# Kernel tuning notes

Hardware: AMD Instinct MI355X
Metric: run time of the kernel (lower is better)

## Reference

```python
import jax, jax.numpy as jnp
import numpy as np
from jax import lax

K = 3; KK = K * K; S = 1; P = 1; D = 1
BN_EPS = 1e-5


def setup_inputs() -> dict:
    key = jax.random.key(0)
    ks = jax.random.split(key, 4)
    B, C, H, W = 8, 128, 64, 64
    cout = 128
    # xavier-ish scales for conv weights
    def xavier(k, shape):
        fan_in = shape[1] * shape[2] * shape[3]
        fan_out = shape[0] * shape[2] * shape[3]
        limit = np.sqrt(6.0 / (fan_in + fan_out))
        return jax.random.uniform(k, shape, jnp.float32, -limit, limit)
    return {
        "x": jax.random.normal(ks[0], (B, C, H, W), jnp.float32),
        "w_off": xavier(ks[1], (2 * KK, C, K, K)),
        "b_off": jnp.zeros((2 * KK,), jnp.float32),
        "w_mod": xavier(ks[2], (KK, C, K, K)),
        "b_mod": jnp.zeros((KK,), jnp.float32),
        "w_reg": xavier(ks[3], (cout, C, K, K)),
        "b_reg": jnp.zeros((cout,), jnp.float32),
        "gamma": jnp.ones((cout,), jnp.float32),
        "beta": jnp.zeros((cout,), jnp.float32),
    }


def _conv(x, w, b):
    y = lax.conv_general_dilated(x, w, (S, S), [(P, P), (P, P)],
                                 rhs_dilation=(D, D),
                                 dimension_numbers=("NCHW", "OIHW", "NCHW"))
    return y + b[None, :, None, None]


def _deform_conv(x, offset, mask, w_reg, b_reg):
    B, C, H, W = x.shape
    Ho, Wo = offset.shape[2], offset.shape[3]
    # torchvision layout: [B, 2*KK, Ho, Wo], interleaved (dy, dx) per tap
    off = offset.reshape(B, KK, 2, Ho, Wo)
    dy, dx = off[:, :, 0], off[:, :, 1]                      # [B,KK,Ho,Wo]
    ki = jnp.arange(KK) // K
    kj = jnp.arange(KK) % K
    base_y = (jnp.arange(Ho) * S - P)[None, :, None] + (ki * D)[:, None, None]  # [KK,Ho,1]
    base_x = (jnp.arange(Wo) * S - P)[None, None, :] + (kj * D)[:, None, None]  # [KK,1,Wo]
    py = base_y[None].astype(x.dtype) + dy                   # [B,KK,Ho,Wo]
    px = base_x[None].astype(x.dtype) + dx

    y0f = jnp.floor(py); x0f = jnp.floor(px)
    ly = py - y0f; lx = px - x0f
    y0 = y0f.astype(jnp.int32); x0 = x0f.astype(jnp.int32)
    y1 = y0 + 1; x1 = x0 + 1

    def gather(iy, ix):
        valid = ((iy >= 0) & (iy < H) & (ix >= 0) & (ix < W)).astype(x.dtype)
        iyc = jnp.clip(iy, 0, H - 1)
        ixc = jnp.clip(ix, 0, W - 1)
        v = jax.vmap(lambda img, a, b: img[:, a, b])(x, iyc, ixc)  # [B,C,KK,Ho,Wo]
        return v * valid[:, None]

    val = (gather(y0, x0) * ((1 - ly) * (1 - lx))[:, None]
           + gather(y0, x1) * ((1 - ly) * lx)[:, None]
           + gather(y1, x0) * (ly * (1 - lx))[:, None]
           + gather(y1, x1) * (ly * lx)[:, None])               # [B,C,KK,Ho,Wo]

    patches = val * mask[:, None]                               # modulated samples
    wr = w_reg.reshape(w_reg.shape[0], C, KK)
    out = jnp.einsum("ock,bckhw->bohw", wr, patches)
    return out + b_reg[None, :, None, None]


def reference(x, w_off, b_off, w_mod, b_mod, w_reg, b_reg, gamma, beta):
    offset = _conv(x, w_off, b_off)
    modulator = 2.0 * jax.nn.sigmoid(_conv(x, w_mod, b_mod))
    y = _deform_conv(x, offset, modulator, w_reg, b_reg)
    # BatchNorm2d (training-mode batch statistics) + ReLU
    mu = y.mean(axis=(0, 2, 3), keepdims=True)
    var = y.var(axis=(0, 2, 3), keepdims=True)
    y = (y - mu) * lax.rsqrt(var + BN_EPS)
    y = y * gamma[None, :, None, None] + beta[None, :, None, None]
    return jax.nn.relu(y)
```

## Files before the change

kernel.cpp:

```cpp
#include <hip/hip_runtime.h>
#include <math.h>

#define H 64
#define W 64
#define C 128
#define NB 8
#define COUT 128
#define HWi 4096

typedef __attribute__((ext_vector_type(8))) short short8;
typedef __attribute__((ext_vector_type(8))) unsigned short ushort8;
typedef __attribute__((ext_vector_type(4))) unsigned short ushort4v;
typedef __attribute__((ext_vector_type(4))) float f32x4;
typedef __attribute__((ext_vector_type(2))) float f32x2;

__device__ __forceinline__ unsigned short f2bf(float f){
    unsigned u = __float_as_uint(f);
    unsigned r = (u + 0x7FFFu + ((u >> 16) & 1u)) >> 16;
    return (unsigned short)r;
}
__device__ __forceinline__ float bf2f(unsigned short u){
    return __uint_as_float(((unsigned)u) << 16);
}
__device__ __forceinline__ f32x2 up2(unsigned p){
    f32x2 r;
    r.x = __uint_as_float(p << 16);
    r.y = __uint_as_float(p & 0xFFFF0000u);
    return r;
}
__device__ __forceinline__ unsigned pk2r(f32x2 v){
    unsigned a = __float_as_uint(v.x) + 0x8000u;
    unsigned b = __float_as_uint(v.y) + 0x8000u;
    return __builtin_amdgcn_perm(b, a, 0x07060302);
}

__global__ void k_pre(const float* __restrict__ x, unsigned short* __restrict__ xTp,
                      const float* __restrict__ w_reg, const float* __restrict__ w_off,
                      const float* __restrict__ w_mod, const float* __restrict__ b_off,
                      const float* __restrict__ b_mod,
                      unsigned short* __restrict__ wAv, unsigned short* __restrict__ w27Av,
                      float* __restrict__ biasom, float* __restrict__ psum){
    int tid = threadIdx.x;
    if (blockIdx.x >= 528){
        int i = (blockIdx.x - 528) * 256 + tid;
        if (i < 147456){
            int kc = i >> 12, rem = i & 4095;
            int t = rem >> 9, ln = (rem >> 3) & 63, j = i & 7;
            int oc = t * 16 + (ln & 15);
            int kkl = ((ln >> 4) << 3) + j;
            int kk = kc * 32 + kkl, k = kk >> 7, c = kk & 127;
            wAv[i] = f2bf(w_reg[oc * 1152 + c * 9 + k]);
        } else if (i < 147456 + 36864){
            int j2 = i - 147456;
            int kc = j2 >> 10, rem = j2 & 1023;
            int mh = rem >> 9, ln = (rem >> 3) & 63, j = j2 & 7;
            int m = mh * 16 + (ln & 15);
            int kkl = ((ln >> 4) << 3) + j;
            int kk = kc * 32 + kkl, k = kk >> 7, c = kk & 127;
            float v = 0.f;
            if (m < 18) v = w_off[m * 1152 + c * 9 + k];
            else if (m < 27) v = w_mod[(m - 18) * 1152 + c * 9 + k];
            w27Av[j2] = f2bf(v);
        } else if (i < 147456 + 36864 + 32){
            int m = i - 147456 - 36864;
            biasom[m] = (m < 18) ? b_off[m] : (m < 27 ? b_mod[m - 18] : 0.f);
        } else if (i < 147456 + 36864 + 32 + 256){
            psum[i - 147456 - 36864 - 32] = 0.f;
        }
        return;
    }
    int bidx = blockIdx.x;
    int b = bidx / 66, hp = bidx - b * 66;
    unsigned short* row = xTp + (size_t)(b * 66 + hp) * 66 * 128;
    if (hp == 0 || hp == 65){
        ushort8 z = {0,0,0,0,0,0,0,0};
        for (int i = tid; i < 66 * 128 / 8; i += 256) ((ushort8*)row)[i] = z;
        return;
    }
    int h = hp - 1;
    __shared__ unsigned s2[64 * 69];
    int w4 = tid & 15, co = tid >> 4;
    #pragma unroll
    for (int p4 = 0; p4 < 4; p4++){
        int c = p4 * 32 + co * 2;
        const float* base = x + (size_t)(b * 128 + c) * HWi + h * 64 + w4 * 4;
        float4 fa = *(const float4*)(base);
        float4 fb = *(const float4*)(base + HWi);
        int c2 = c >> 1;
        s2[(w4 * 4 + 0) * 69 + c2] = (unsigned)f2bf(fa.x) | ((unsigned)f2bf(fb.x) << 16);
        s2[(w4 * 4 + 1) * 69 + c2] = (unsigned)f2bf(fa.y) | ((unsigned)f2bf(fb.y) << 16);
        s2[(w4 * 4 + 2) * 69 + c2] = (unsigned)f2bf(fa.z) | ((unsigned)f2bf(fb.z) << 16);
        s2[(w4 * 4 + 3) * 69 + c2] = (unsigned)f2bf(fa.w) | ((unsigned)f2bf(fb.w) << 16);
    }
    __syncthreads();
    if (tid < 32){
        ushort8 z = {0,0,0,0,0,0,0,0};
        int wp = (tid < 16) ? 0 : 65;
        int sg = tid & 15;
        *(ushort8*)(row + wp * 128 + sg * 8) = z;
    }
    for (int it = tid; it < 1024; it += 256){
        int w2 = it >> 4, sg = it & 15;
        uint4 v;
        v.x = s2[w2 * 69 + sg * 4 + 0];
        v.y = s2[w2 * 69 + sg * 4 + 1];
        v.z = s2[w2 * 69 + sg * 4 + 2];
        v.w = s2[w2 * 69 + sg * 4 + 3];
        *(uint4*)(row + (w2 + 1) * 128 + sg * 8) = v;
    }
}

__global__ __launch_bounds__(256) void k_main(const unsigned short* __restrict__ xTp,
        const unsigned short* __restrict__ wAv, const unsigned short* __restrict__ w27Av,
        const float* __restrict__ biasom, const float* __restrict__ b_reg,
        unsigned short* __restrict__ ybf, float* __restrict__ psum){
    __shared__ char smem[33536];
    float* s_om = (float*)smem;
    int*   s_a4 = (int*)(smem + 8448);
    float* s_w4 = (float*)(smem + 17664);

    int tid = threadIdx.x;
    int n0 = blockIdx.x * 64;
    int b = n0 >> 12, h = (n0 >> 6) & 63;
    int wv = tid >> 6, lane = tid & 63, quad = lane >> 4, l16 = lane & 15;
    int px0 = wv * 16;

    {
        f32x4 accA = {0.f,0.f,0.f,0.f}, accB = {0.f,0.f,0.f,0.f};
        #pragma unroll
        for (int k9 = 0; k9 < 9; k9++){
            int ki = k9 / 3, kj = k9 - ki * 3;
            const unsigned short* brow =
                xTp + (size_t)((b * 66 + h + ki) * 66 + px0 + l16 + kj) * 128 + quad * 8;
            #pragma unroll
            for (int c4 = 0; c4 < 4; c4++){
                int kc = k9 * 4 + c4;
                short8 bO = *(const short8*)(brow + c4 * 32);
                short8 a0 = *(const short8*)(w27Av + kc * 1024 + lane * 8);
                short8 a1 = *(const short8*)(w27Av + kc * 1024 + 512 + lane * 8);
                accA = __builtin_amdgcn_mfma_f32_16x16x32_bf16(a0, bO, accA, 0, 0, 0);
                accB = __builtin_amdgcn_mfma_f32_16x16x32_bf16(a1, bO, accB, 0, 0, 0);
            }
        }
        int pxl = px0 + l16;
        #pragma unroll
        for (int r = 0; r < 4; r++){
            int ch = quad * 4 + r;
            s_om[pxl * 33 + ch] = accA[r] + biasom[ch];
        }
        #pragma unroll
        for (int r = 0; r < 4; r++){
            int ch = 16 + quad * 4 + r;
            if (ch < 27){
                float v = accB[r] + biasom[ch];
                if (ch >= 18) v = 2.f / (1.f + expf(-v));
                s_om[pxl * 33 + ch] = v;
            }
        }
    }
    __syncthreads();

    for (int idx = tid; idx < 576; idx += 256){
        int k = idx >> 6, px = idx & 63;
        float dy = s_om[px * 33 + 2 * k];
        float dx = s_om[px * 33 + 2 * k + 1];
        float m  = s_om[px * 33 + 18 + k];
        int ki = k / 3, kj = k - ki * 3;
        float py  = (float)(h - 1 + ki) + dy;
        float pxf = (float)(px - 1 + kj) + dx;
        float y0f = floorf(py), x0f = floorf(pxf);
        float ly = py - y0f, lx = pxf - x0f;
        int iy0 = (int)y0f, ix0 = (int)x0f;
        int cy0 = min(max(iy0 + 1, 0), 65), cy1 = min(max(iy0 + 2, 0), 65);
        int cx0 = min(max(ix0 + 1, 0), 65), cx1 = min(max(ix0 + 2, 0), 65);
        int rb = b * 66 * 66;
        int4 ca;
        ca.x = ((rb + cy0 * 66) + cx0) * 128;
        ca.y = ((rb + cy0 * 66) + cx1) * 128;
        ca.z = ((rb + cy1 * 66) + cx0) * 128;
        ca.w = ((rb + cy1 * 66) + cx1) * 128;
        float4 cw;
        cw.x = (1.f - ly) * (1.f - lx) * m;
        cw.y = (1.f - ly) * lx * m;
        cw.z = ly * (1.f - lx) * m;
        cw.w = ly * lx * m;
        *(int4*)(s_a4 + idx * 4)   = ca;
        *(float4*)(s_w4 + idx * 4) = cw;
    }
    __syncthreads();

    int px = px0 + l16;
    int cq = quad;

    f32x4 acc[8];
    #pragma unroll
    for (int t = 0; t < 8; t++) acc[t] = (f32x4){0.f,0.f,0.f,0.f};

    int4 ca; float4 cw, wS;
    short8 aC[8], aN[8];
    ushort8 cC[4], cN[4];

    {
        int i0 = px * 4;
        ca = *(const int4*)(s_a4 + i0);
        cw = *(const float4*)(s_w4 + i0);
        wS = cw;
        const unsigned short* ab = wAv + lane * 8;
        #pragma unroll
        for (int t = 0; t < 8; t++) aC[t] = *(const short8*)(ab + t * 512);
        int co = cq * 8;
        cC[0] = *(const ushort8*)(xTp + ca.x + co);
        cC[1] = *(const ushort8*)(xTp + ca.y + co);
        cC[2] = *(const ushort8*)(xTp + ca.z + co);
        cC[3] = *(const ushort8*)(xTp + ca.w + co);
    }

    #pragma unroll 4
    for (int kc = 0; kc < 36; kc++){
        short8 bfr;
        {
            unsigned* op = (unsigned*)&bfr;
            const unsigned* u0 = (const unsigned*)&cC[0];
            const unsigned* u1 = (const unsigned*)&cC[1];
            const unsigned* u2 = (const unsigned*)&cC[2];
            const unsigned* u3 = (const unsigned*)&cC[3];
            #pragma unroll
            for (int j = 0; j < 4; j++){
                f32x2 v = wS.x * up2(u0[j]);
                v += wS.y * up2(u1[j]);
                v += wS.z * up2(u2[j]);
                v += wS.w * up2(u3[j]);
                op[j] = pk2r(v);
            }
        }
        if (kc + 1 < 36){
            if (((kc + 1) & 3) == 0){
                int i0 = (((kc + 1) >> 2) * 64 + px) * 4;
                ca = *(const int4*)(s_a4 + i0);
                cw = *(const float4*)(s_w4 + i0);
            }
            int co = ((kc + 1) & 3) * 32 + cq * 8;
            cN[0] = *(const ushort8*)(xTp + ca.x + co);
            cN[1] = *(const ushort8*)(xTp + ca.y + co);
            cN[2] = *(const ushort8*)(xTp + ca.z + co);
            cN[3] = *(const ushort8*)(xTp + ca.w + co);
            const unsigned short* ab = wAv + (kc + 1) * 4096 + lane * 8;
            #pragma unroll
            for (int t = 0; t < 8; t++) aN[t] = *(const short8*)(ab + t * 512);
        }
        #pragma unroll
        for (int t = 0; t < 8; t++)
            acc[t] = __builtin_amdgcn_mfma_f32_16x16x32_bf16(aC[t], bfr, acc[t], 0, 0, 0);
        #pragma unroll
        for (int t = 0; t < 8; t++) aC[t] = aN[t];
        cC[0] = cN[0]; cC[1] = cN[1]; cC[2] = cN[2]; cC[3] = cN[3];
        wS = cw;
    }

    __syncthreads();
    float* ls = (float*)smem;
    int sp0 = h * 64;
    #pragma unroll
    for (int t = 0; t < 8; t++){
        #pragma unroll
        for (int r = 0; r < 4; r++){
            int oc = t * 16 + quad * 4 + r;
            float v = acc[t][r] + b_reg[oc];
            ybf[(size_t)(b * 128 + oc) * HWi + sp0 + px] = f2bf(v);
            ls[oc * 65 + px] = v;
        }
    }
    __syncthreads();
    if (tid < 128){
        int oc = tid;
        float s = 0.f, s2 = 0.f;
        #pragma unroll 8
        for (int nl = 0; nl < 64; nl++){
            float v = ls[oc * 65 + nl];
            s += v; s2 = fmaf(v, v, s2);
        }
        atomicAdd(&psum[oc], s);
        atomicAdd(&psum[128 + oc], s2);
    }
}

__global__ void k_apply(const unsigned short* __restrict__ ybf, const float* __restrict__ psum,
                        const float* __restrict__ gamma, const float* __restrict__ beta,
                        float* __restrict__ out){
    int e8 = (blockIdx.x * 256 + threadIdx.x) * 8;
    int c = (e8 >> 12) & 127;
    ushort8 u = *(const ushort8*)(ybf + e8);
    float s = psum[c], s2 = psum[128 + c];
    float mean = s * (1.f / 32768.f);
    float var  = s2 * (1.f / 32768.f) - mean * mean;
    float rs = rsqrtf(var + 1e-5f);
    float g = gamma[c] * rs;
    float bt = beta[c] - mean * g;
    float4 lo, hi;
    lo.x = fmaxf(fmaf(bf2f(u[0]), g, bt), 0.f);
    lo.y = fmaxf(fmaf(bf2f(u[1]), g, bt), 0.f);
    lo.z = fmaxf(fmaf(bf2f(u[2]), g, bt), 0.f);
    lo.w = fmaxf(fmaf(bf2f(u[3]), g, bt), 0.f);
    hi.x = fmaxf(fmaf(bf2f(u[4]), g, bt), 0.f);
    hi.y = fmaxf(fmaf(bf2f(u[5]), g, bt), 0.f);
    hi.z = fmaxf(fmaf(bf2f(u[6]), g, bt), 0.f);
    hi.w = fmaxf(fmaf(bf2f(u[7]), g, bt), 0.f);
    *(float4*)(out + e8)     = lo;
    *(float4*)(out + e8 + 4) = hi;
}

extern "C" void kernel_launch(void* const* d_in, const int* in_sizes, int n_in,
                              void* d_out, int out_size, void* d_ws, size_t ws_size,
                              hipStream_t stream){
    const float* x     = (const float*)d_in[0];
    const float* w_off = (const float*)d_in[1];
    const float* b_off = (const float*)d_in[2];
    const float* w_mod = (const float*)d_in[3];
    const float* b_mod = (const float*)d_in[4];
    const float* w_reg = (const float*)d_in[5];
    const float* b_reg = (const float*)d_in[6];
    const float* gamma = (const float*)d_in[7];
    const float* beta  = (const float*)d_in[8];

    char* wsb = (char*)d_ws;
    unsigned short* xTp   = (unsigned short*)(wsb);
    unsigned short* ybf   = (unsigned short*)(wsb + 8921088);
    unsigned short* wAv   = (unsigned short*)(wsb + 17309696);
    unsigned short* w27Av = (unsigned short*)(wsb + 17604608);
    float*          biasom= (float*)(wsb + 17678336);
    float*          psum  = (float*)(wsb + 17678464);
    float* out = (float*)d_out;

    hipLaunchKernelGGL(k_pre,   dim3(1250), dim3(256), 0, stream, x, xTp, w_reg, w_off, w_mod, b_off, b_mod, wAv, w27Av, biasom, psum);
    hipLaunchKernelGGL(k_main,  dim3(512),  dim3(256), 0, stream, xTp, wAv, w27Av, biasom, b_reg, ybf, psum);
    hipLaunchKernelGGL(k_apply, dim3(2048), dim3(256), 0, stream, ybf, psum, gamma, beta, out);
}
```

Measured before the change: 162.6 us.

## Split deformable GEMM reduction across two waves per pixel group

Doubles the k_main block to 512 threads, pairing two waves per 16-pixel group. Each wave in a pair handles half of the 36 K-chunks of the deformable conv GEMM and one half of the offset/mask conv output channels. Partial accumulators are combined through shared memory before bias, the bf16 store and the BN partial sums. The aim is more waves per CU to hide gather latency, at the cost of an extra LDS reduction, another barrier and higher register pressure under the new launch bounds.

Measured after the change: 177.7 us. 1.09x slower.

```diff
diff --git a/kernel.cpp b/kernel.cpp
--- a/kernel.cpp
+++ b/kernel.cpp
@@ -110,11 +110,11 @@
     }
 }
 
-__global__ __launch_bounds__(256) void k_main(const unsigned short* __restrict__ xTp,
+__global__ __launch_bounds__(512) void k_main(const unsigned short* __restrict__ xTp,
         const unsigned short* __restrict__ wAv, const unsigned short* __restrict__ w27Av,
         const float* __restrict__ biasom, const float* __restrict__ b_reg,
         unsigned short* __restrict__ ybf, float* __restrict__ psum){
-    __shared__ char smem[33536];
+    __shared__ __align__(16) char smem[34816];
     float* s_om = (float*)smem;
     int*   s_a4 = (int*)(smem + 8448);
     float* s_w4 = (float*)(smem + 17664);
@@ -123,10 +123,11 @@
     int n0 = blockIdx.x * 64;
     int b = n0 >> 12, h = (n0 >> 6) & 63;
     int wv = tid >> 6, lane = tid & 63, quad = lane >> 4, l16 = lane & 15;
-    int px0 = wv * 16;
+    int g = wv >> 1, s = wv & 1;
+    int px0 = g * 16;
 
     {
-        f32x4 accA = {0.f,0.f,0.f,0.f}, accB = {0.f,0.f,0.f,0.f};
+        f32x4 accO = {0.f,0.f,0.f,0.f};
         #pragma unroll
         for (int k9 = 0; k9 < 9; k9++){
             int ki = k9 / 3, kj = k9 - ki * 3;
@@ -136,23 +137,16 @@
             for (int c4 = 0; c4 < 4; c4++){
                 int kc = k9 * 4 + c4;
                 short8 bO = *(const short8*)(brow + c4 * 32);
-                short8 a0 = *(const short8*)(w27Av + kc * 1024 + lane * 8);
-                short8 a1 = *(const short8*)(w27Av + kc * 1024 + 512 + lane * 8);
-                accA = __builtin_amdgcn_mfma_f32_16x16x32_bf16(a0, bO, accA, 0, 0, 0);
-                accB = __builtin_amdgcn_mfma_f32_16x16x32_bf16(a1, bO, accB, 0, 0, 0);
+                short8 aO = *(const short8*)(w27Av + kc * 1024 + s * 512 + lane * 8);
+                accO = __builtin_amdgcn_mfma_f32_16x16x32_bf16(aO, bO, accO, 0, 0, 0);
             }
         }
         int pxl = px0 + l16;
         #pragma unroll
         for (int r = 0; r < 4; r++){
-            int ch = quad * 4 + r;
-            s_om[pxl * 33 + ch] = accA[r] + biasom[ch];
-        }
-        #pragma unroll
-        for (int r = 0; r < 4; r++){
-            int ch = 16 + quad * 4 + r;
+            int ch = s * 16 + quad * 4 + r;
             if (ch < 27){
-                float v = accB[r] + biasom[ch];
+                float v = accO[r] + biasom[ch];
                 if (ch >= 18) v = 2.f / (1.f + expf(-v));
                 s_om[pxl * 33 + ch] = v;
             }
@@ -160,7 +154,7 @@
     }
     __syncthreads();
 
-    for (int idx = tid; idx < 576; idx += 256){
+    for (int idx = tid; idx < 576; idx += 512){
         int k = idx >> 6, px = idx & 63;
         float dy = s_om[px * 33 + 2 * k];
         float dx = s_om[px * 33 + 2 * k + 1];
@@ -191,6 +185,7 @@
 
     int px = px0 + l16;
     int cq = quad;
+    int kc0 = s * 18, kc1 = kc0 + 18;
 
     f32x4 acc[8];
     #pragma unroll
@@ -201,22 +196,22 @@
     ushort8 cC[4], cN[4];
 
     {
-        int i0 = px * 4;
+        int i0 = ((kc0 >> 2) * 64 + px) * 4;
         ca = *(const int4*)(s_a4 + i0);
         cw = *(const float4*)(s_w4 + i0);
         wS = cw;
-        const unsigned short* ab = wAv + lane * 8;
+        const unsigned short* ab = wAv + kc0 * 4096 + lane * 8;
         #pragma unroll
         for (int t = 0; t < 8; t++) aC[t] = *(const short8*)(ab + t * 512);
-        int co = cq * 8;
+        int co = (kc0 & 3) * 32 + cq * 8;
         cC[0] = *(const ushort8*)(xTp + ca.x + co);
         cC[1] = *(const ushort8*)(xTp + ca.y + co);
         cC[2] = *(const ushort8*)(xTp + ca.z + co);
         cC[3] = *(const ushort8*)(xTp + ca.w + co);
     }
 
-    #pragma unroll 4
-    for (int kc = 0; kc < 36; kc++){
+    #pragma unroll 2
+    for (int kc = kc0; kc < kc1; kc++){
         short8 bfr;
         {
             unsigned* op = (unsigned*)&bfr;
@@ -233,7 +228,7 @@
                 op[j] = pk2r(v);
             }
         }
-        if (kc + 1 < 36){
+        if (kc + 1 < kc1){
             if (((kc + 1) & 3) == 0){
                 int i0 = (((kc + 1) >> 2) * 64 + px) * 4;
                 ca = *(const int4*)(s_a4 + i0);
@@ -258,28 +253,45 @@
     }
 
     __syncthreads();
-    float* ls = (float*)smem;
-    int sp0 = h * 64;
-    #pragma unroll
-    for (int t = 0; t < 8; t++){
-        #pragma unroll
-        for (int r = 0; r < 4; r++){
-            int oc = t * 16 + quad * 4 + r;
-            float v = acc[t][r] + b_reg[oc];
-            ybf[(size_t)(b * 128 + oc) * HWi + sp0 + px] = f2bf(v);
-            ls[oc * 65 + px] = v;
+    float* lsE = (float*)smem;
+    int baseg = g * (128 * 17);
+    if (s == 0){
+        #pragma unroll
+        for (int t = 0; t < 8; t++){
+            #pragma unroll
+            for (int r = 0; r < 4; r++){
+                int oc = t * 16 + quad * 4 + r;
+                lsE[baseg + oc * 17 + l16] = acc[t][r];
+            }
+        }
+    }
+    __syncthreads();
+    if (s == 1){
+        int sp0 = h * 64;
+        #pragma unroll
+        for (int t = 0; t < 8; t++){
+            #pragma unroll
+            for (int r = 0; r < 4; r++){
+                int oc = t * 16 + quad * 4 + r;
+                float v = acc[t][r] + lsE[baseg + oc * 17 + l16] + b_reg[oc];
+                ybf[(size_t)(b * 128 + oc) * HWi + sp0 + px] = f2bf(v);
+                lsE[baseg + oc * 17 + l16] = v;
+            }
         }
     }
     __syncthreads();
     if (tid < 128){
         int oc = tid;
-        float s = 0.f, s2 = 0.f;
-        #pragma unroll 8
-        for (int nl = 0; nl < 64; nl++){
-            float v = ls[oc * 65 + nl];
-            s += v; s2 = fmaf(v, v, s2);
-        }
-        atomicAdd(&psum[oc], s);
+        float sm = 0.f, s2 = 0.f;
+        #pragma unroll
+        for (int g2 = 0; g2 < 4; g2++){
+            #pragma unroll 4
+            for (int p = 0; p < 16; p++){
+                float v = lsE[g2 * (128 * 17) + oc * 17 + p];
+                sm += v; s2 = fmaf(v, v, s2);
+            }
+        }
+        atomicAdd(&psum[oc], sm);
         atomicAdd(&psum[128 + oc], s2);
     }
 }
@@ -332,6 +344,6 @@
     float* out = (float*)d_out;
 
     hipLaunchKernelGGL(k_pre,   dim3(1250), dim3(256), 0, stream, x, xTp, w_reg, w_off, w_mod, b_off, b_mod, wAv, w27Av, biasom, psum);
-    hipLaunchKernelGGL(k_main,  dim3(512),  dim3(256), 0, stream, xTp, wAv, w27Av, biasom, b_reg, ybf, psum);
+    hipLaunchKernelGGL(k_main,  dim3(512),  dim3(512), 0, stream, xTp, wAv, w27Av, biasom, b_reg, ybf, psum);
     hipLaunchKernelGGL(k_apply, dim3(2048), dim3(256), 0, stream, ybf, psum, gamma, beta, out);
 }
```
